# Optimization experiments

Hardware: AMD Instinct MI355X
Metric: run time of the kernel (lower is better)

## Reference

```python
import jax, jax.numpy as jnp
import numpy as np

B, S, HIDDEN = 2, 2048, 1024
HEADS, HEAD_DIM = 16, 64
GRID_SIZE, SPLINE_ORDER = 5, 3  # efficient-kan defaults


def b_splines(x, grid, k=SPLINE_ORDER):
    """x: (N, in), grid: (in, GRID_SIZE + 2k + 1) -> (N, in, GRID_SIZE + k)."""
    xe = x[..., None]
    bases = ((xe >= grid[:, :-1]) & (xe < grid[:, 1:])).astype(x.dtype)
    for p in range(1, k + 1):  # Cox-de Boor recursion, fixed small loop
        left = (xe - grid[:, : -(p + 1)]) / (grid[:, p:-1] - grid[:, : -(p + 1)]) * bases[..., :-1]
        right = (grid[:, p + 1:] - xe) / (grid[:, p + 1:] - grid[:, 1:-p]) * bases[..., 1:]
        bases = left + right
    return bases


def setup_inputs() -> dict:
    key = jax.random.key(0)
    ks = jax.random.split(key, 7)
    h = 2.0 / GRID_SIZE  # grid_range = [-1, 1]
    grid_1d = (jnp.arange(-SPLINE_ORDER, GRID_SIZE + SPLINE_ORDER + 1, dtype=jnp.float32) * h - 1.0)
    grid = jnp.tile(grid_1d[None, :], (HIDDEN, 1))  # (in, 12)
    return {
        "x": jax.random.normal(ks[0], (B, S, HIDDEN), jnp.float32),
        "base_weight": jax.random.normal(ks[1], (3 * HIDDEN, HIDDEN), jnp.float32) * 0.02,
        "spline_weight": jax.random.normal(ks[2], (3 * HIDDEN, HIDDEN, GRID_SIZE + SPLINE_ORDER), jnp.float32) * 0.02,
        "spline_scaler": jax.random.normal(ks[3], (3 * HIDDEN, HIDDEN), jnp.float32) * 0.1 + 1.0,
        "grid": grid,
        "rotation_matrix": jax.random.normal(ks[4], (HEAD_DIM, HEAD_DIM), jnp.float32) / np.sqrt(HEAD_DIM),
        "out_w": jax.random.normal(ks[5], (HIDDEN, HIDDEN), jnp.float32) * 0.02,
        "out_b": jnp.zeros((HIDDEN,), jnp.float32),
    }


def reference(x, base_weight, spline_weight, spline_scaler, grid, rotation_matrix, out_w, out_b):
    Bc, Sc, Hc = x.shape
    xf = x.reshape(-1, Hc)  # (N, in)
    # KANLinear: silu base branch + B-spline branch
    base = jax.nn.silu(xf) @ base_weight.T  # (N, 3H)
    bs = b_splines(xf, grid)  # (N, in, G+k)
    sw = spline_weight * spline_scaler[..., None]  # scaled spline weight
    spline = bs.reshape(bs.shape[0], -1) @ sw.reshape(sw.shape[0], -1).T
    qkv = (base + spline).reshape(Bc, Sc, HEADS, 3 * HEAD_DIM).transpose(0, 2, 1, 3)
    q, k, v = jnp.split(qkv, 3, axis=-1)  # each (B,H,S,dh)
    # RoPE via full learned rotation matrix
    qr = jnp.einsum('bhsd,md->bhsm', q, rotation_matrix)
    kr = jnp.einsum('bhsd,md->bhsm', k, rotation_matrix)
    scores = jnp.einsum('bhsm,bhtm->bhst', qr, kr) / (HEAD_DIM ** 0.5)
    attn = jax.nn.softmax(scores, axis=-1)
    ctx = jnp.einsum('bhst,bhtd->bhsd', attn, v)
    ctx = ctx.transpose(0, 2, 1, 3).reshape(Bc, Sc, Hc)
    return ctx @ out_w.T + out_b
```

## Files before the change

### kernel.cpp

```cpp
#include <hip/hip_runtime.h>
#include <cstdint>
#include <cstddef>

typedef __bf16 bf16;
typedef bf16  bf16x8 __attribute__((ext_vector_type(8)));
typedef float f32x4  __attribute__((ext_vector_type(4)));

#define GLOBAL_AS __attribute__((address_space(1)))
#define LDS_AS    __attribute__((address_space(3)))

__device__ __forceinline__ void ldg_lds16(const void* g, void* l) {
  __builtin_amdgcn_global_load_lds((const GLOBAL_AS void*)g, (LDS_AS void*)l, 16, 0, 0);
}

constexpr int NB    = 2;
constexpr int SQ    = 2048;
constexpr int HID   = 1024;
constexpr int NHEAD = 16;
constexpr int HD    = 64;
constexpr int NROW  = NB * SQ;
constexpr int KA    = HID + HID * 8;
constexpr int NO    = 3 * HID;

__global__ __launch_bounds__(256) void build_a(const float* __restrict__ X,
                                               const float* __restrict__ Grid,
                                               bf16* __restrict__ A) {
  int idx = blockIdx.x * 256 + threadIdx.x;
  int n = idx >> 10, i = idx & 1023;
  float x = X[idx];
  float s = x / (1.0f + __expf(-x));
  A[(size_t)n * KA + i] = (bf16)s;

  float kn[12];
#pragma unroll
  for (int t = 0; t < 12; t++) kn[t] = Grid[i * 12 + t];
  float bs[11];
#pragma unroll
  for (int t = 0; t < 11; t++) bs[t] = (x >= kn[t] && x < kn[t + 1]) ? 1.0f : 0.0f;
#pragma unroll
  for (int p = 1; p <= 3; p++) {
#pragma unroll
    for (int t = 0; t + p < 11; t++) {
      bs[t] = (x - kn[t]) / (kn[t + p] - kn[t]) * bs[t]
            + (kn[t + p + 1] - x) / (kn[t + p + 1] - kn[t + 1]) * bs[t + 1];
    }
  }
  union { bf16 h[8]; uint4 u; } pk;
#pragma unroll
  for (int t = 0; t < 8; t++) pk.h[t] = (bf16)bs[t];
  *(uint4*)(A + (size_t)n * KA + HID + i * 8) = pk.u;
}

__global__ __launch_bounds__(256) void build_w(const float* __restrict__ BW,
                                               const float* __restrict__ SW,
                                               const float* __restrict__ SS,
                                               bf16* __restrict__ Wp) {
  int idx = blockIdx.x * 256 + threadIdx.x;
  int o = idx / 1152;
  int jc = idx - o * 1152;
  float4 f0, f1;
  if (jc < 128) {
    f0 = *(const float4*)(BW + (size_t)o * HID + jc * 8);
    f1 = *(const float4*)(BW + (size_t)o * HID + jc * 8 + 4);
  } else {
    int ii = jc - 128;
    float sc = SS[(size_t)o * HID + ii];
    f0 = *(const float4*)(SW + ((size_t)o * HID + ii) * 8);
    f1 = *(const float4*)(SW + ((size_t)o * HID + ii) * 8 + 4);
    f0.x *= sc; f0.y *= sc; f0.z *= sc; f0.w *= sc;
    f1.x *= sc; f1.y *= sc; f1.z *= sc; f1.w *= sc;
  }
  union { bf16 h[8]; uint4 u; } pk;
  pk.h[0] = (bf16)f0.x; pk.h[1] = (bf16)f0.y; pk.h[2] = (bf16)f0.z; pk.h[3] = (bf16)f0.w;
  pk.h[4] = (bf16)f1.x; pk.h[5] = (bf16)f1.y; pk.h[6] = (bf16)f1.z; pk.h[7] = (bf16)f1.w;
  *(uint4*)(Wp + (size_t)o * KA + jc * 8) = pk.u;
}

__global__ __launch_bounds__(256) void conv_wout(const float* __restrict__ OW,
                                                 bf16* __restrict__ WOB) {
  int i = (blockIdx.x * 256 + threadIdx.x) * 4;
  float4 f = *(const float4*)(OW + i);
  union { bf16 h[4]; uint2 u; } p;
  p.h[0] = (bf16)f.x; p.h[1] = (bf16)f.y; p.h[2] = (bf16)f.z; p.h[3] = (bf16)f.w;
  *(uint2*)(WOB + i) = p.u;
}

__global__ __launch_bounds__(256) void compute_m(const float* __restrict__ R,
                                                 bf16* __restrict__ Mb) {
  __shared__ float Rl[64 * 64];
  int tid = threadIdx.x;
  for (int idx = tid; idx < 4096; idx += 256) Rl[idx] = R[idx];
  __syncthreads();
  int d = tid >> 2;
  int e0 = (tid & 3) * 16;
#pragma unroll
  for (int j = 0; j < 16; j++) {
    int e = e0 + j;
    float acc = 0.f;
#pragma unroll
    for (int m = 0; m < 64; m++) acc += Rl[m * 64 + d] * Rl[m * 64 + e];
    Mb[d * 64 + e] = (bf16)(0.125f * acc);
  }
}

template <int K>
__device__ __forceinline__ void gemm_tile(const bf16* __restrict__ A,
                                          const bf16* __restrict__ Bw,
                                          int rowBase, int colBase,
                                          bf16* As, bf16* Bs, f32x4 acc[4][4]) {
  const int tid  = threadIdx.x;
  const int lane = tid & 63, wave = tid >> 6;
  const int wm = (wave >> 1) * 64, wn = (wave & 1) * 64;
  const int l15 = lane & 15, quad = lane >> 4;
  const int rA = tid >> 2;
  const int swSrc = ((tid & 3) ^ ((rA >> 1) & 3)) * 8;
  const int swRd  = (quad ^ ((l15 >> 1) & 3)) * 8;
#pragma unroll
  for (int mi = 0; mi < 4; mi++)
#pragma unroll
    for (int ni = 0; ni < 4; ni++) acc[mi][ni] = (f32x4){0.f, 0.f, 0.f, 0.f};

  const bf16* Ag1 = A  + (size_t)(rowBase + rA) * K + swSrc;
  const bf16* Ag2 = A  + (size_t)(rowBase + 64 + rA) * K + swSrc;
  const bf16* Bg1 = Bw + (size_t)(colBase + rA) * K + swSrc;
  const bf16* Bg2 = Bw + (size_t)(colBase + 64 + rA) * K + swSrc;

  for (int k0 = 0; k0 < K; k0 += 32) {
    __syncthreads();
    ldg_lds16(Ag1 + k0, As + tid * 8);
    ldg_lds16(Ag2 + k0, As + 2048 + tid * 8);
    ldg_lds16(Bg1 + k0, Bs + tid * 8);
    ldg_lds16(Bg2 + k0, Bs + 2048 + tid * 8);
    __syncthreads();
    bf16x8 af[4], bfr[4];
#pragma unroll
    for (int mi = 0; mi < 4; mi++)
      af[mi] = *(const bf16x8*)(As + (wm + mi * 16 + l15) * 32 + swRd);
#pragma unroll
    for (int ni = 0; ni < 4; ni++)
      bfr[ni] = *(const bf16x8*)(Bs + (wn + ni * 16 + l15) * 32 + swRd);
#pragma unroll
    for (int mi = 0; mi < 4; mi++)
#pragma unroll
      for (int ni = 0; ni < 4; ni++)
        acc[mi][ni] = __builtin_amdgcn_mfma_f32_16x16x32_bf16(af[mi], bfr[ni], acc[mi][ni], 0, 0, 0);
  }
}

__global__ __launch_bounds__(512, 2) void gemm_qkv(const bf16* __restrict__ A,
                                                   const bf16* __restrict__ W,
                                                   bf16* __restrict__ QQ,
                                                   bf16* __restrict__ KK,
                                                   bf16* __restrict__ VV) {
  constexpr int BM = 256, BN = 192, BK = 64;
  constexpr int NT = KA / BK;
  __shared__ __align__(16) bf16 As[2 * BM * BK];
  __shared__ __align__(16) bf16 Bs[2 * BN * BK];
  const int tid  = threadIdx.x;
  const int lane = tid & 63, wave = tid >> 6;
  const int wr = wave >> 2, wc = wave & 3;
  const int l15 = lane & 15, quad = lane >> 4;
  const int xw = l15 & 7;
  const int rowBase = blockIdx.y * BM;
  const int colBase = blockIdx.x * BN;

  int aRow[4], aOff[4];
#pragma unroll
  for (int i = 0; i < 4; i++) {
    int c = i * 512 + tid;
    aRow[i] = c >> 3;
    aOff[i] = ((c & 7) ^ (aRow[i] & 7)) * 8;
  }
  int bRow[3], bOff[3];
#pragma unroll
  for (int i = 0; i < 3; i++) {
    int c = i * 512 + tid;
    bRow[i] = c >> 3;
    bOff[i] = ((c & 7) ^ (bRow[i] & 7)) * 8;
  }
  const int dstBase = tid * 8;

  auto stage = [&](int t, int b) {
    const bf16* Asrc = A + (size_t)rowBase * KA + (size_t)t * BK;
    const bf16* Bsrc = W + (size_t)colBase * KA + (size_t)t * BK;
    bf16* Ad = As + b * (BM * BK);
    bf16* Bd = Bs + b * (BN * BK);
#pragma unroll
    for (int i = 0; i < 4; i++)
      ldg_lds16(Asrc + (size_t)aRow[i] * KA + aOff[i], Ad + i * 4096 + dstBase);
#pragma unroll
    for (int i = 0; i < 3; i++)
      ldg_lds16(Bsrc + (size_t)bRow[i] * KA + bOff[i], Bd + i * 4096 + dstBase);
  };

  f32x4 acc[8][3];
#pragma unroll
  for (int mi = 0; mi < 8; mi++)
#pragma unroll
    for (int nj = 0; nj < 3; nj++) acc[mi][nj] = (f32x4){0.f, 0.f, 0.f, 0.f};

  stage(0, 0);
  stage(1, 1);
  asm volatile("s_waitcnt vmcnt(7)\n\ts_barrier" ::: "memory");

  auto tile_step = [&](int t, int b) {
    const bf16* Ab = As + b * (BM * BK);
    const bf16* Bb = Bs + b * (BN * BK);
    bf16x8 af[2][8], bfv[2][3];
#pragma unroll
    for (int kc = 0; kc < 2; kc++) {
      const int slot = ((kc * 4 + quad) ^ xw) * 8;
#pragma unroll
      for (int mi = 0; mi < 8; mi++)
        af[kc][mi] = *(const bf16x8*)(Ab + (wr * 128 + mi * 16 + l15) * 64 + slot);
#pragma unroll
      for (int nj = 0; nj < 3; nj++)
        bfv[kc][nj] = *(const bf16x8*)(Bb + (wc * 48 + nj * 16 + l15) * 64 + slot);
    }
    __builtin_amdgcn_s_setprio(1);
#pragma unroll
    for (int mi = 0; mi < 8; mi++)
#pragma unroll
      for (int nj = 0; nj < 3; nj++)
        acc[mi][nj] = __builtin_amdgcn_mfma_f32_16x16x32_bf16(af[0][mi], bfv[0][nj], acc[mi][nj], 0, 0, 0);
    __builtin_amdgcn_s_setprio(0);
    asm volatile("s_waitcnt lgkmcnt(0)\n\ts_barrier" ::: "memory");
    if (t + 2 < NT) stage(t + 2, b);
    __builtin_amdgcn_s_setprio(1);
#pragma unroll
    for (int mi = 0; mi < 8; mi++)
#pragma unroll
      for (int nj = 0; nj < 3; nj++)
        acc[mi][nj] = __builtin_amdgcn_mfma_f32_16x16x32_bf16(af[1][mi], bfv[1][nj], acc[mi][nj], 0, 0, 0);
    __builtin_amdgcn_s_setprio(0);
    if (t + 2 < NT)
      asm volatile("s_waitcnt vmcnt(7)\n\ts_barrier" ::: "memory");
    else
      asm volatile("s_waitcnt vmcnt(0)\n\ts_barrier" ::: "memory");
  };

#pragma unroll 1
  for (int t = 0; t < NT; t += 2) {
    tile_step(t, 0);
    tile_step(t + 1, 1);
  }

  const int h = blockIdx.x;
#pragma unroll
  for (int mi = 0; mi < 8; mi++)
#pragma unroll
    for (int nj = 0; nj < 3; nj++)
#pragma unroll
      for (int r = 0; r < 4; r++) {
        int row = rowBase + wr * 128 + mi * 16 + quad * 4 + r;
        int c = wc * 48 + nj * 16 + l15;
        int b = row >> 11, s = row & 2047;
        size_t base = ((size_t)(b * NHEAD + h) * SQ + s) * HD;
        float v = acc[mi][nj][r];
        if (c < 64)        QQ[base + c] = (bf16)v;
        else if (c < 128)  KK[base + c - 64] = (bf16)v;
        else               VV[base + c - 128] = (bf16)v;
      }
}

__global__ __launch_bounds__(256) void transpose_v(const bf16* __restrict__ VV,
                                                   bf16* __restrict__ VT) {
  __shared__ __align__(16) bf16 Ts[64 * 72];
  const int st = blockIdx.x, bh = blockIdx.y, tid = threadIdx.x;
  const bf16* src = VV + ((size_t)bh * SQ + st * 64) * HD;
#pragma unroll
  for (int i = 0; i < 2; i++) {
    int c = i * 256 + tid, row = c >> 3, seg = c & 7;
    bf16x8 v8 = *(const bf16x8*)(src + row * HD + seg * 8);
    *(bf16x8*)(&Ts[row * 72 + seg * 8]) = v8;
  }
  __syncthreads();
#pragma unroll
  for (int i = 0; i < 2; i++) {
    int c = i * 256 + tid, drow = c >> 3, seg = c & 7;
    bf16x8 o8;
#pragma unroll
    for (int j = 0; j < 8; j++) o8[j] = Ts[(seg * 8 + j) * 72 + drow];
    *(bf16x8*)(VT + ((size_t)bh * HD + drow) * SQ + st * 64 + seg * 8) = o8;
  }
}

__global__ __launch_bounds__(256) void attn(const bf16* __restrict__ QQ,
                                            const bf16* __restrict__ KK,
                                            const bf16* __restrict__ VT,
                                            const bf16* __restrict__ Mb,
                                            bf16* __restrict__ CTXB) {
  __shared__ __align__(16) bf16 Qs[128 * 64];
  __shared__ __align__(16) bf16 Ks[128 * 64];
  __shared__ __align__(16) bf16 Vt[64 * 128];
  __shared__ __align__(16) bf16 Ps[128 * 64];
  __shared__ __align__(16) bf16 Ms[64 * 64];
  const int bh = blockIdx.y;
  const int b = bh >> 4, h = bh & 15;
  const int qbase = blockIdx.x * 128;
  const bf16* Q  = QQ + (size_t)bh * SQ * HD;
  const bf16* Kp = KK + (size_t)bh * SQ * HD;
  const bf16* Vp = VT + (size_t)bh * HD * SQ;
  const int tid = threadIdx.x, lane = tid & 63, wave = tid >> 6;
  const int l15 = lane & 15, quad = lane >> 4;
  const int sw8 = l15 & 7;
  const float SHIFT = 12.0f;

#pragma unroll
  for (int i = 0; i < 4; i++) {
    int c = i * 256 + tid, row = c >> 3, seg = c & 7;
    ldg_lds16(Q + (size_t)(qbase + row) * HD + ((seg ^ (row & 7)) * 8), Qs + c * 8);
  }
#pragma unroll
  for (int i = 0; i < 2; i++) {
    int c = i * 256 + tid, row = c >> 3, seg = c & 7;
    ldg_lds16(Mb + row * 64 + ((seg ^ (row & 7)) * 8), Ms + c * 8);
  }
  __syncthreads();

  {
    f32x4 racc[2][4];
#pragma unroll
    for (int mi = 0; mi < 2; mi++)
#pragma unroll
      for (int nj = 0; nj < 4; nj++) racc[mi][nj] = (f32x4){0.f, 0.f, 0.f, 0.f};
#pragma unroll
    for (int kc = 0; kc < 2; kc++) {
      const int slot = ((kc * 4 + quad) ^ sw8) * 8;
      bf16x8 aq[2], bm[4];
#pragma unroll
      for (int mi = 0; mi < 2; mi++)
        aq[mi] = *(const bf16x8*)(Qs + (wave * 32 + mi * 16 + l15) * 64 + slot);
#pragma unroll
      for (int nj = 0; nj < 4; nj++)
        bm[nj] = *(const bf16x8*)(Ms + (nj * 16 + l15) * 64 + slot);
#pragma unroll
      for (int mi = 0; mi < 2; mi++)
#pragma unroll
        for (int nj = 0; nj < 4; nj++)
          racc[mi][nj] = __builtin_amdgcn_mfma_f32_16x16x32_bf16(aq[mi], bm[nj], racc[mi][nj], 0, 0, 0);
    }
#pragma unroll
    for (int mi = 0; mi < 2; mi++)
#pragma unroll
      for (int nj = 0; nj < 4; nj++)
#pragma unroll
        for (int r = 0; r < 4; r++) {
          int qrow = wave * 32 + mi * 16 + quad * 4 + r;
          int slot = ((nj * 2 + (l15 >> 3)) ^ (qrow & 7)) * 8 + (l15 & 7);
          Qs[qrow * 64 + slot] = (bf16)racc[mi][nj][r];
        }
  }
  bf16x8 qf[2][2];
#pragma unroll
  for (int kc = 0; kc < 2; kc++)
#pragma unroll
    for (int mi = 0; mi < 2; mi++)
      qf[mi][kc] = *(const bf16x8*)(Qs + (wave * 32 + mi * 16 + l15) * 64 + (((kc * 4 + quad) ^ sw8) * 8));

  float lpart[2][4];
  f32x4 ctxacc[2][4];
#pragma unroll
  for (int mi = 0; mi < 2; mi++)
#pragma unroll
    for (int r = 0; r < 4; r++) lpart[mi][r] = 0.f;
#pragma unroll
  for (int mi = 0; mi < 2; mi++)
#pragma unroll
    for (int nd = 0; nd < 4; nd++) ctxacc[mi][nd] = (f32x4){0.f, 0.f, 0.f, 0.f};

  for (int kt = 0; kt < SQ / 128; kt++) {
    const int kbase = kt * 128;
    if (kt) __syncthreads();
#pragma unroll
    for (int i = 0; i < 4; i++) {
      int c = i * 256 + tid, row = c >> 3, seg = c & 7;
      ldg_lds16(Kp + (size_t)(kbase + row) * HD + ((seg ^ (row & 7)) * 8), Ks + c * 8);
    }
#pragma unroll
    for (int i = 0; i < 4; i++) {
      int c = i * 256 + tid, row = c >> 4, seg = c & 15;
      ldg_lds16(Vp + (size_t)row * SQ + kbase + ((seg ^ (row & 7)) * 8), Vt + c * 8);
    }
    __syncthreads();

#pragma unroll
    for (int hh = 0; hh < 2; hh++) {
      f32x4 sacc[2][4];
#pragma unroll
      for (int mi = 0; mi < 2; mi++)
#pragma unroll
        for (int nj = 0; nj < 4; nj++) sacc[mi][nj] = (f32x4){0.f, 0.f, 0.f, 0.f};
#pragma unroll
      for (int kc = 0; kc < 2; kc++) {
        const int slot = ((kc * 4 + quad) ^ sw8) * 8;
        bf16x8 bfr[4];
#pragma unroll
        for (int nj = 0; nj < 4; nj++)
          bfr[nj] = *(const bf16x8*)(Ks + (hh * 64 + nj * 16 + l15) * 64 + slot);
#pragma unroll
        for (int mi = 0; mi < 2; mi++)
#pragma unroll
          for (int nj = 0; nj < 4; nj++)
            sacc[mi][nj] = __builtin_amdgcn_mfma_f32_16x16x32_bf16(qf[mi][kc], bfr[nj], sacc[mi][nj], 0, 0, 0);
      }
#pragma unroll
      for (int mi = 0; mi < 2; mi++)
#pragma unroll
        for (int nj = 0; nj < 4; nj++)
#pragma unroll
          for (int r = 0; r < 4; r++) {
            float p = __expf(sacc[mi][nj][r] - SHIFT);
            lpart[mi][r] += p;
            int prow = wave * 32 + mi * 16 + quad * 4 + r;
            int slot = ((nj * 2 + (l15 >> 3)) ^ (prow & 7)) * 8 + (l15 & 7);
            Ps[prow * 64 + slot] = (bf16)p;
          }
#pragma unroll
      for (int kc = 0; kc < 2; kc++) {
        const int aslot = ((kc * 4 + quad) ^ sw8) * 8;
        const int vslot = (((hh * 8 + kc * 4 + quad)) ^ sw8) * 8;
        bf16x8 af[2], bfr[4];
#pragma unroll
        for (int mi = 0; mi < 2; mi++)
          af[mi] = *(const bf16x8*)(Ps + (wave * 32 + mi * 16 + l15) * 64 + aslot);
#pragma unroll
        for (int nd = 0; nd < 4; nd++)
          bfr[nd] = *(const bf16x8*)(Vt + (nd * 16 + l15) * 128 + vslot);
#pragma unroll
        for (int mi = 0; mi < 2; mi++)
#pragma unroll
          for (int nd = 0; nd < 4; nd++)
            ctxacc[mi][nd] = __builtin_amdgcn_mfma_f32_16x16x32_bf16(af[mi], bfr[nd], ctxacc[mi][nd], 0, 0, 0);
      }
    }
  }

#pragma unroll
  for (int mi = 0; mi < 2; mi++)
#pragma unroll
    for (int r = 0; r < 4; r++) {
      float l = lpart[mi][r];
#pragma unroll
      for (int off = 1; off < 16; off <<= 1) l += __shfl_xor(l, off);
      float inv = 1.0f / l;
#pragma unroll
      for (int nd = 0; nd < 4; nd++) {
        int srow = qbase + wave * 32 + mi * 16 + quad * 4 + r;
        float val = ctxacc[mi][nd][r] * inv;
        CTXB[(size_t)(b * SQ + srow) * HID + h * HD + nd * 16 + l15] = (bf16)val;
      }
    }
}

__global__ __launch_bounds__(256) void gemm_out(const bf16* __restrict__ CTX,
                                                const bf16* __restrict__ WOB,
                                                const float* __restrict__ OB,
                                                float* __restrict__ OUT) {
  __shared__ __align__(16) bf16 As[128 * 32];
  __shared__ __align__(16) bf16 Bs[128 * 32];
  f32x4 acc[4][4];
  const int rowBase = blockIdx.y * 128, colBase = blockIdx.x * 128;
  gemm_tile<HID>(CTX, WOB, rowBase, colBase, As, Bs, acc);

  const int tid = threadIdx.x, lane = tid & 63, wave = tid >> 6;
  const int wm = (wave >> 1) * 64, wn = (wave & 1) * 64;
  const int l15 = lane & 15, quad = lane >> 4;
#pragma unroll
  for (int mi = 0; mi < 4; mi++)
#pragma unroll
    for (int ni = 0; ni < 4; ni++)
#pragma unroll
      for (int r = 0; r < 4; r++) {
        int row = rowBase + wm + mi * 16 + quad * 4 + r;
        int col = colBase + wn + ni * 16 + l15;
        OUT[(size_t)row * HID + col] = acc[mi][ni][r] + OB[col];
      }
}

extern "C" void kernel_launch(void* const* d_in, const int* in_sizes, int n_in,
                              void* d_out, int out_size, void* d_ws, size_t ws_size,
                              hipStream_t stream) {
  const float* x    = (const float*)d_in[0];
  const float* bw   = (const float*)d_in[1];
  const float* sw   = (const float*)d_in[2];
  const float* ss   = (const float*)d_in[3];
  const float* grid = (const float*)d_in[4];
  const float* rot  = (const float*)d_in[5];
  const float* ow   = (const float*)d_in[6];
  const float* ob   = (const float*)d_in[7];
  float* out = (float*)d_out;

  char* ws = (char*)d_ws;
  bf16* Aact = (bf16*)(ws);
  bf16* vt   = (bf16*)(ws);
  bf16* Mb   = (bf16*)(ws + 8388608);
  bf16* Wp   = (bf16*)(ws + 75497472);
  bf16* qq   = (bf16*)(ws + 132120576);
  bf16* kk   = (bf16*)(ws + 140509184);
  bf16* vv   = (bf16*)(ws + 148897792);
  bf16* ctxb = (bf16*)(ws + 157286400);
  bf16* wob  = (bf16*)(ws + 165675008);

  build_a<<<NROW * HID / 256, 256, 0, stream>>>(x, grid, Aact);
  build_w<<<NO * (KA / 8) / 256, 256, 0, stream>>>(bw, sw, ss, Wp);
  conv_wout<<<HID * HID / 1024, 256, 0, stream>>>(ow, wob);
  gemm_qkv<<<dim3(NO / 192, NROW / 256), 512, 0, stream>>>(Aact, Wp, qq, kk, vv);
  compute_m<<<1, 256, 0, stream>>>(rot, Mb);
  transpose_v<<<dim3(SQ / 64, NB * NHEAD), 256, 0, stream>>>(vv, vt);
  attn<<<dim3(SQ / 128, NB * NHEAD), 256, 0, stream>>>(qq, kk, vt, Mb, ctxb);
  gemm_out<<<dim3(HID / 128, NROW / 128), 256, 0, stream>>>(ctxb, wob, ob, out);
}
```

Measured before the change: 645.1 us.

## Split QKV GEMM main loop into four barrier-synchronized MFMA sub-phases

Restructures the QKV GEMM inner loop so each K-tile is processed in four 12-MFMA sub-phases, with LDS fragment reads interleaved between them instead of one bulk read up front. Global-to-LDS staging is split into two groups: the A chunks read later are prefetched one tile ahead, and the remaining A chunks plus B are prefetched two tiles ahead. The aim is to hide LDS reads and global loads behind MFMA work and to lower register pressure from holding all fragments at once. The cost is many more s_barrier instructions per tile, whose synchronization overhead may outweigh the added overlap.

```diff
diff --git a/kernel.cpp b/kernel.cpp
--- a/kernel.cpp
+++ b/kernel.cpp
@@ -147,6 +147,32 @@
   }
 }
 
+#define RD_A(dst, H, KC)                                                       \
+  {                                                                            \
+    _Pragma("unroll") for (int i_ = 0; i_ < 4; i_++)                           \
+        dst[i_] = *(const bf16x8*)(Ab +                                        \
+            (wr * 128 + ((H) * 4 + i_) * 16 + l15) * 64 +                      \
+            ((((KC) * 4 + quad) ^ xw) * 8));                                   \
+  }
+
+#define RD_B(dst, KC)                                                          \
+  {                                                                            \
+    _Pragma("unroll") for (int j_ = 0; j_ < 3; j_++)                           \
+        dst[j_] = *(const bf16x8*)(Bb +                                        \
+            (wc * 48 + j_ * 16 + l15) * 64 +                                   \
+            ((((KC) * 4 + quad) ^ xw) * 8));                                   \
+  }
+
+#define MM12(afr, bfr, H)                                                      \
+  {                                                                            \
+    __builtin_amdgcn_s_setprio(1);                                             \
+    _Pragma("unroll") for (int i_ = 0; i_ < 4; i_++)                           \
+        _Pragma("unroll") for (int j_ = 0; j_ < 3; j_++)                       \
+            acc[(H) * 4 + i_][j_] = __builtin_amdgcn_mfma_f32_16x16x32_bf16(   \
+                afr[i_], bfr[j_], acc[(H) * 4 + i_][j_], 0, 0, 0);             \
+    __builtin_amdgcn_s_setprio(0);                                             \
+  }
+
 __global__ __launch_bounds__(512, 2) void gemm_qkv(const bf16* __restrict__ A,
                                                    const bf16* __restrict__ W,
                                                    bf16* __restrict__ QQ,
@@ -180,17 +206,22 @@
   }
   const int dstBase = tid * 8;
 
-  auto stage = [&](int t, int b) {
+  auto stageA1 = [&](int t) {
+    const bf16* Asrc = A + (size_t)rowBase * KA + (size_t)t * BK;
+    bf16* Ad = As + (t & 1) * (BM * BK);
+    ldg_lds16(Asrc + (size_t)aRow[1] * KA + aOff[1], Ad + 1 * 4096 + dstBase);
+    ldg_lds16(Asrc + (size_t)aRow[3] * KA + aOff[3], Ad + 3 * 4096 + dstBase);
+  };
+  auto stageA0B = [&](int t) {
     const bf16* Asrc = A + (size_t)rowBase * KA + (size_t)t * BK;
     const bf16* Bsrc = W + (size_t)colBase * KA + (size_t)t * BK;
-    bf16* Ad = As + b * (BM * BK);
-    bf16* Bd = Bs + b * (BN * BK);
-#pragma unroll
-    for (int i = 0; i < 4; i++)
-      ldg_lds16(Asrc + (size_t)aRow[i] * KA + aOff[i], Ad + i * 4096 + dstBase);
-#pragma unroll
-    for (int i = 0; i < 3; i++)
-      ldg_lds16(Bsrc + (size_t)bRow[i] * KA + bOff[i], Bd + i * 4096 + dstBase);
+    bf16* Ad = As + (t & 1) * (BM * BK);
+    bf16* Bd = Bs + (t & 1) * (BN * BK);
+    ldg_lds16(Asrc + (size_t)aRow[0] * KA + aOff[0], Ad + 0 * 4096 + dstBase);
+    ldg_lds16(Asrc + (size_t)aRow[2] * KA + aOff[2], Ad + 2 * 4096 + dstBase);
+    ldg_lds16(Bsrc + (size_t)bRow[0] * KA + bOff[0], Bd + 0 * 4096 + dstBase);
+    ldg_lds16(Bsrc + (size_t)bRow[1] * KA + bOff[1], Bd + 1 * 4096 + dstBase);
+    ldg_lds16(Bsrc + (size_t)bRow[2] * KA + bOff[2], Bd + 2 * 4096 + dstBase);
   };
 
   f32x4 acc[8][3];
@@ -199,50 +230,44 @@
 #pragma unroll
     for (int nj = 0; nj < 3; nj++) acc[mi][nj] = (f32x4){0.f, 0.f, 0.f, 0.f};
 
-  stage(0, 0);
-  stage(1, 1);
-  asm volatile("s_waitcnt vmcnt(7)\n\ts_barrier" ::: "memory");
-
-  auto tile_step = [&](int t, int b) {
-    const bf16* Ab = As + b * (BM * BK);
-    const bf16* Bb = Bs + b * (BN * BK);
-    bf16x8 af[2][8], bfv[2][3];
-#pragma unroll
-    for (int kc = 0; kc < 2; kc++) {
-      const int slot = ((kc * 4 + quad) ^ xw) * 8;
-#pragma unroll
-      for (int mi = 0; mi < 8; mi++)
-        af[kc][mi] = *(const bf16x8*)(Ab + (wr * 128 + mi * 16 + l15) * 64 + slot);
-#pragma unroll
-      for (int nj = 0; nj < 3; nj++)
-        bfv[kc][nj] = *(const bf16x8*)(Bb + (wc * 48 + nj * 16 + l15) * 64 + slot);
-    }
-    __builtin_amdgcn_s_setprio(1);
-#pragma unroll
-    for (int mi = 0; mi < 8; mi++)
-#pragma unroll
-      for (int nj = 0; nj < 3; nj++)
-        acc[mi][nj] = __builtin_amdgcn_mfma_f32_16x16x32_bf16(af[0][mi], bfv[0][nj], acc[mi][nj], 0, 0, 0);
-    __builtin_amdgcn_s_setprio(0);
-    asm volatile("s_waitcnt lgkmcnt(0)\n\ts_barrier" ::: "memory");
-    if (t + 2 < NT) stage(t + 2, b);
-    __builtin_amdgcn_s_setprio(1);
-#pragma unroll
-    for (int mi = 0; mi < 8; mi++)
-#pragma unroll
-      for (int nj = 0; nj < 3; nj++)
-        acc[mi][nj] = __builtin_amdgcn_mfma_f32_16x16x32_bf16(af[1][mi], bfv[1][nj], acc[mi][nj], 0, 0, 0);
-    __builtin_amdgcn_s_setprio(0);
-    if (t + 2 < NT)
-      asm volatile("s_waitcnt vmcnt(7)\n\ts_barrier" ::: "memory");
-    else
+  stageA0B(0);
+  stageA1(0);
+  stageA0B(1);
+  asm volatile("s_waitcnt vmcnt(5)\n\ts_barrier" ::: "memory");
+
+#pragma unroll 1
+  for (int t = 0; t < NT; t++) {
+    const bf16* Ab = As + (t & 1) * (BM * BK);
+    const bf16* Bb = Bs + (t & 1) * (BN * BK);
+    bf16x8 a0[4], a1[4], b0[3], b1[3];
+    RD_A(a0, 0, 0);
+    RD_B(b0, 0);
+    if (t + 1 < NT) stageA1(t + 1);
+    __builtin_amdgcn_s_barrier();
+    asm volatile("s_waitcnt lgkmcnt(0)" ::: "memory");
+    MM12(a0, b0, 0);
+    __builtin_amdgcn_s_barrier();
+    RD_A(a1, 1, 0);
+    __builtin_amdgcn_s_barrier();
+    asm volatile("s_waitcnt lgkmcnt(0)" ::: "memory");
+    MM12(a1, b0, 1);
+    __builtin_amdgcn_s_barrier();
+    RD_A(a0, 0, 1);
+    RD_B(b1, 1);
+    __builtin_amdgcn_s_barrier();
+    asm volatile("s_waitcnt lgkmcnt(0)" ::: "memory");
+    MM12(a0, b1, 0);
+    __builtin_amdgcn_s_barrier();
+    RD_A(a1, 1, 1);
+    if (t + 2 < NT) stageA0B(t + 2);
+    __builtin_amdgcn_s_barrier();
+    asm volatile("s_waitcnt lgkmcnt(0)" ::: "memory");
+    MM12(a1, b1, 1);
+    if (t + 2 < NT) {
+      asm volatile("s_waitcnt vmcnt(5)\n\ts_barrier" ::: "memory");
+    } else {
       asm volatile("s_waitcnt vmcnt(0)\n\ts_barrier" ::: "memory");
-  };
-
-#pragma unroll 1
-  for (int t = 0; t < NT; t += 2) {
-    tile_step(t, 0);
-    tile_step(t + 1, 1);
+    }
   }
 
   const int h = blockIdx.x;
```

New measurement: 681.3 us. 5.6% more time.

## Double-buffer K/V tiles in attention and remap blocks for XCD locality

Applied to the files above, without the earlier changes.

The attention kernel now uses 64-key tiles with two LDS buffers. The next K/V tile is prefetched with async global-to-LDS loads while the current tile is computed, and each step ends in a single waitcnt+barrier instead of two syncs per 128-key tile. The launch also becomes a 1D grid of 512 blocks whose index is remapped so that blocks for the same (batch, head) are grouped, which is meant to improve L2 reuse of K/V across the chiplets. The risk is that the single barrier may not cover the Ps write/read hazard between iterations, and the smaller tiles add more loop-iteration overhead.

```diff
diff --git a/kernel.cpp b/kernel.cpp
--- a/kernel.cpp
+++ b/kernel.cpp
@@ -290,14 +290,18 @@
                                             const bf16* __restrict__ VT,
                                             const bf16* __restrict__ Mb,
                                             bf16* __restrict__ CTXB) {
+  constexpr int NKT = SQ / 64;
   __shared__ __align__(16) bf16 Qs[128 * 64];
-  __shared__ __align__(16) bf16 Ks[128 * 64];
-  __shared__ __align__(16) bf16 Vt[64 * 128];
+  __shared__ __align__(16) bf16 Ks[2 * 64 * 64];
+  __shared__ __align__(16) bf16 Vt[2 * 64 * 64];
   __shared__ __align__(16) bf16 Ps[128 * 64];
   __shared__ __align__(16) bf16 Ms[64 * 64];
-  const int bh = blockIdx.y;
+  const int id  = blockIdx.x;
+  const int sub = id >> 3;
+  const int bh  = (id & 7) * 4 + (sub >> 4);
+  const int qi  = sub & 15;
   const int b = bh >> 4, h = bh & 15;
-  const int qbase = blockIdx.x * 128;
+  const int qbase = qi * 128;
   const bf16* Q  = QQ + (size_t)bh * SQ * HD;
   const bf16* Kp = KK + (size_t)bh * SQ * HD;
   const bf16* Vp = VT + (size_t)bh * HD * SQ;
@@ -306,6 +310,22 @@
   const int sw8 = l15 & 7;
   const float SHIFT = 12.0f;
 
+  auto stageKV = [&](int kt2, int bufsel) {
+    const int kb = kt2 * 64;
+#pragma unroll
+    for (int i = 0; i < 2; i++) {
+      int c = i * 256 + tid, row = c >> 3, seg = c & 7;
+      ldg_lds16(Kp + (size_t)(kb + row) * HD + ((seg ^ (row & 7)) * 8),
+                Ks + bufsel * 4096 + c * 8);
+    }
+#pragma unroll
+    for (int i = 0; i < 2; i++) {
+      int c = i * 256 + tid, row = c >> 3, seg = c & 7;
+      ldg_lds16(Vp + (size_t)row * SQ + kb + ((seg ^ (row & 7)) * 8),
+                Vt + bufsel * 4096 + c * 8);
+    }
+  };
+
 #pragma unroll
   for (int i = 0; i < 4; i++) {
     int c = i * 256 + tid, row = c >> 3, seg = c & 7;
@@ -316,6 +336,7 @@
     int c = i * 256 + tid, row = c >> 3, seg = c & 7;
     ldg_lds16(Mb + row * 64 + ((seg ^ (row & 7)) * 8), Ms + c * 8);
   }
+  stageKV(0, 0);
   __syncthreads();
 
   {
@@ -369,71 +390,60 @@
 #pragma unroll
     for (int nd = 0; nd < 4; nd++) ctxacc[mi][nd] = (f32x4){0.f, 0.f, 0.f, 0.f};
 
-  for (int kt = 0; kt < SQ / 128; kt++) {
-    const int kbase = kt * 128;
-    if (kt) __syncthreads();
-#pragma unroll
-    for (int i = 0; i < 4; i++) {
-      int c = i * 256 + tid, row = c >> 3, seg = c & 7;
-      ldg_lds16(Kp + (size_t)(kbase + row) * HD + ((seg ^ (row & 7)) * 8), Ks + c * 8);
-    }
-#pragma unroll
-    for (int i = 0; i < 4; i++) {
-      int c = i * 256 + tid, row = c >> 4, seg = c & 15;
-      ldg_lds16(Vp + (size_t)row * SQ + kbase + ((seg ^ (row & 7)) * 8), Vt + c * 8);
-    }
-    __syncthreads();
-
-#pragma unroll
-    for (int hh = 0; hh < 2; hh++) {
-      f32x4 sacc[2][4];
+#pragma unroll 1
+  for (int kt = 0; kt < NKT; kt++) {
+    const int buf = kt & 1;
+    const bf16* Kb = Ks + buf * 4096;
+    const bf16* Vb = Vt + buf * 4096;
+    if (kt + 1 < NKT) stageKV(kt + 1, buf ^ 1);
+
+    f32x4 sacc[2][4];
+#pragma unroll
+    for (int mi = 0; mi < 2; mi++)
+#pragma unroll
+      for (int nj = 0; nj < 4; nj++) sacc[mi][nj] = (f32x4){0.f, 0.f, 0.f, 0.f};
+#pragma unroll
+    for (int kc = 0; kc < 2; kc++) {
+      const int slot = ((kc * 4 + quad) ^ sw8) * 8;
+      bf16x8 bfr[4];
+#pragma unroll
+      for (int nj = 0; nj < 4; nj++)
+        bfr[nj] = *(const bf16x8*)(Kb + (nj * 16 + l15) * 64 + slot);
 #pragma unroll
       for (int mi = 0; mi < 2; mi++)
 #pragma unroll
-        for (int nj = 0; nj < 4; nj++) sacc[mi][nj] = (f32x4){0.f, 0.f, 0.f, 0.f};
-#pragma unroll
-      for (int kc = 0; kc < 2; kc++) {
-        const int slot = ((kc * 4 + quad) ^ sw8) * 8;
-        bf16x8 bfr[4];
-#pragma unroll
         for (int nj = 0; nj < 4; nj++)
-          bfr[nj] = *(const bf16x8*)(Ks + (hh * 64 + nj * 16 + l15) * 64 + slot);
-#pragma unroll
-        for (int mi = 0; mi < 2; mi++)
-#pragma unroll
-          for (int nj = 0; nj < 4; nj++)
-            sacc[mi][nj] = __builtin_amdgcn_mfma_f32_16x16x32_bf16(qf[mi][kc], bfr[nj], sacc[mi][nj], 0, 0, 0);
-      }
+          sacc[mi][nj] = __builtin_amdgcn_mfma_f32_16x16x32_bf16(qf[mi][kc], bfr[nj], sacc[mi][nj], 0, 0, 0);
+    }
+#pragma unroll
+    for (int mi = 0; mi < 2; mi++)
+#pragma unroll
+      for (int nj = 0; nj < 4; nj++)
+#pragma unroll
+        for (int r = 0; r < 4; r++) {
+          float p = __expf(sacc[mi][nj][r] - SHIFT);
+          lpart[mi][r] += p;
+          int prow = wave * 32 + mi * 16 + quad * 4 + r;
+          int slot = ((nj * 2 + (l15 >> 3)) ^ (prow & 7)) * 8 + (l15 & 7);
+          Ps[prow * 64 + slot] = (bf16)p;
+        }
+#pragma unroll
+    for (int kc = 0; kc < 2; kc++) {
+      const int slot = ((kc * 4 + quad) ^ sw8) * 8;
+      bf16x8 af[2], bfr[4];
 #pragma unroll
       for (int mi = 0; mi < 2; mi++)
-#pragma unroll
-        for (int nj = 0; nj < 4; nj++)
-#pragma unroll
-          for (int r = 0; r < 4; r++) {
-            float p = __expf(sacc[mi][nj][r] - SHIFT);
-            lpart[mi][r] += p;
-            int prow = wave * 32 + mi * 16 + quad * 4 + r;
-            int slot = ((nj * 2 + (l15 >> 3)) ^ (prow & 7)) * 8 + (l15 & 7);
-            Ps[prow * 64 + slot] = (bf16)p;
-          }
-#pragma unroll
-      for (int kc = 0; kc < 2; kc++) {
-        const int aslot = ((kc * 4 + quad) ^ sw8) * 8;
-        const int vslot = (((hh * 8 + kc * 4 + quad)) ^ sw8) * 8;
-        bf16x8 af[2], bfr[4];
-#pragma unroll
-        for (int mi = 0; mi < 2; mi++)
-          af[mi] = *(const bf16x8*)(Ps + (wave * 32 + mi * 16 + l15) * 64 + aslot);
+        af[mi] = *(const bf16x8*)(Ps + (wave * 32 + mi * 16 + l15) * 64 + slot);
+#pragma unroll
+      for (int nd = 0; nd < 4; nd++)
+        bfr[nd] = *(const bf16x8*)(Vb + (nd * 16 + l15) * 64 + slot);
+#pragma unroll
+      for (int mi = 0; mi < 2; mi++)
 #pragma unroll
         for (int nd = 0; nd < 4; nd++)
-          bfr[nd] = *(const bf16x8*)(Vt + (nd * 16 + l15) * 128 + vslot);
-#pragma unroll
-        for (int mi = 0; mi < 2; mi++)
-#pragma unroll
-          for (int nd = 0; nd < 4; nd++)
-            ctxacc[mi][nd] = __builtin_amdgcn_mfma_f32_16x16x32_bf16(af[mi], bfr[nd], ctxacc[mi][nd], 0, 0, 0);
-      }
-    }
+          ctxacc[mi][nd] = __builtin_amdgcn_mfma_f32_16x16x32_bf16(af[mi], bfr[nd], ctxacc[mi][nd], 0, 0, 0);
+    }
+    asm volatile("s_waitcnt vmcnt(0)\n\ts_barrier" ::: "memory");
   }
 
 #pragma unroll
@@ -508,6 +518,6 @@
   gemm_qkv<<<dim3(NO / 192, NROW / 256), 512, 0, stream>>>(Aact, Wp, qq, kk, vv);
   compute_m<<<1, 256, 0, stream>>>(rot, Mb);
   transpose_v<<<dim3(SQ / 64, NB * NHEAD), 256, 0, stream>>>(vv, vt);
-  attn<<<dim3(SQ / 128, NB * NHEAD), 256, 0, stream>>>(qq, kk, vt, Mb, ctxb);
+  attn<<<512, 256, 0, stream>>>(qq, kk, vt, Mb, ctxb);
   gemm_out<<<dim3(HID / 128, NROW / 128), 256, 0, stream>>>(ctxb, wob, ob, out);
 }
```

Result: no change. 639.4 us (-0.9%).
